# Kernel tuning notes

Measured on AMD Instinct MI355X. Metric: run time of the kernel, lower is better.

The kernel has to match this reference:

```python
import jax, jax.numpy as jnp
import numpy as np
import math

B, T, D = 2, 4096, 1024
H = 16
HEAD_DIM = D // H
CHUNK = 64

def setup_inputs() -> dict:
    key = jax.random.key(0)
    ks = jax.random.split(key, 9)
    s = 1.0 / math.sqrt(D)
    return {
        'x':  jax.random.normal(ks[0], (B, T, D), dtype=jnp.float32),
        'Wq': jax.random.normal(ks[1], (D, D), dtype=jnp.float32) * s,
        'bq': jax.random.normal(ks[2], (D,), dtype=jnp.float32) * 0.01,
        'Wk': jax.random.normal(ks[3], (D, D), dtype=jnp.float32) * s,
        'bk': jax.random.normal(ks[4], (D,), dtype=jnp.float32) * 0.01,
        'Wv': jax.random.normal(ks[5], (D, D), dtype=jnp.float32) * s,
        'bv': jax.random.normal(ks[6], (D,), dtype=jnp.float32) * 0.01,
        'Wo': jax.random.normal(ks[7], (D, D), dtype=jnp.float32) * s,
        'bo': jax.random.normal(ks[8], (D,), dtype=jnp.float32) * 0.01,
    }

def chunked_attention(q, k, v, chunk_size, scale):
    # q,k,v: (B,H,T,hd); causal Q-chunked attention, chunk_size divides T
    Bq, Hq, Tq, hd = q.shape
    S = k.shape[2]
    nc = Tq // chunk_size
    # (nc, B, H, chunk, hd)
    q_chunks = q.reshape(Bq, Hq, nc, chunk_size, hd).transpose(2, 0, 1, 3, 4)
    starts = jnp.arange(nc, dtype=jnp.int32) * chunk_size
    k_pos = jnp.arange(S)

    def body(carry, xs):
        qc, start = xs  # qc: (B,H,chunk,hd)
        scores = jnp.einsum('bhqd,bhkd->bhqk', qc, k) * scale  # (B,H,chunk,S)
        q_pos = start + jnp.arange(chunk_size)
        causal_mask = k_pos[None, :] > q_pos[:, None]  # (chunk,S)
        scores = jnp.where(causal_mask[None, None], -jnp.inf, scores)
        m = jnp.max(scores, axis=-1, keepdims=True)
        m = jnp.where(jnp.isinf(m), jnp.zeros_like(m), m)
        p = jax.nn.softmax(scores - m, axis=-1)
        oc = jnp.einsum('bhqk,bhkd->bhqd', p, v)
        return carry, oc

    _, outs = jax.lax.scan(body, None, (q_chunks, starts))  # (nc,B,H,chunk,hd)
    return outs.transpose(1, 2, 0, 3, 4).reshape(Bq, Hq, Tq, hd)

def reference(x, Wq, bq, Wk, bk, Wv, bv, Wo, bo):
    Bx, Tx, Dx = x.shape
    scale = 1.0 / math.sqrt(HEAD_DIM)

    def proj(W, b):
        y = x @ W.T + b  # torch Linear convention
        return y.reshape(Bx, Tx, H, HEAD_DIM).transpose(0, 2, 1, 3)

    q = proj(Wq, bq)
    k = proj(Wk, bk)
    v = proj(Wv, bv)
    out = chunked_attention(q, k, v, CHUNK, scale)  # (B,H,T,hd)
    out = out.transpose(0, 2, 1, 3).reshape(Bx, Tx, Dx)
    return out @ Wo.T + bo
```

## Files before the change

kernel.cpp:

```cpp
#include <hip/hip_runtime.h>
#include <math.h>

#define B_  2
#define T_  4096
#define D_  1024
#define H_  16
#define HD_ 64
#define M_  8192

using f32x4  = __attribute__((ext_vector_type(4)))  float;
using f32x16 = __attribute__((ext_vector_type(16))) float;
using bfrag  = __attribute__((ext_vector_type(8)))  short;

__device__ __forceinline__ unsigned short f2bf(float f) {
  union { float f; unsigned u; } v; v.f = f;
  unsigned r = v.u + 0x7FFFu + ((v.u >> 16) & 1u);
  return (unsigned short)(r >> 16);
}

__device__ __forceinline__ unsigned cvt_pk(float lo, float hi) {
  unsigned r;
  asm("v_cvt_pk_bf16_f32 %0, %1, %2" : "=v"(r) : "v"(lo), "v"(hi));
  return r;
}

__device__ __forceinline__ void plswap(unsigned &a, unsigned &b) {
  asm("v_permlane32_swap_b32 %0, %1" : "+v"(a), "+v"(b));
}

__device__ __forceinline__ void async16(const void* g, void* l) {
  __builtin_amdgcn_global_load_lds(
      (const __attribute__((address_space(1))) unsigned int*)g,
      (__attribute__((address_space(3))) unsigned int*)l, 16, 0, 0);
}

__global__ __launch_bounds__(256) void convert_all(
    const float* __restrict__ x, const float* __restrict__ wq,
    const float* __restrict__ wk, const float* __restrict__ wv,
    const float* __restrict__ wo, unsigned short* __restrict__ dst)
{
  const size_t NX = (size_t)M_ * D_ / 4;
  const size_t NW = (size_t)D_ * D_ / 4;
  const size_t total = NX + 4 * NW;
  size_t i = (size_t)blockIdx.x * blockDim.x + threadIdx.x;
  size_t stride = (size_t)gridDim.x * blockDim.x;
  for (size_t v = i; v < total; v += stride) {
    const float4* src;
    if (v < NX) {
      src = (const float4*)x + v;
    } else {
      size_t j = v - NX;
      const float* wp = (j < NW) ? wq : (j < 2*NW) ? wk : (j < 3*NW) ? wv : wo;
      src = (const float4*)wp + (j & (NW - 1));
    }
    float4 f = *src;
    ushort4 u;
    u.x = f2bf(f.x); u.y = f2bf(f.y); u.z = f2bf(f.z); u.w = f2bf(f.w);
    *(ushort4*)(dst + v * 4) = u;
  }
}

__global__ __launch_bounds__(256) void gemm_qkv(
    const unsigned short* __restrict__ A,
    const unsigned short* __restrict__ Ww,
    const float* __restrict__ bq, const float* __restrict__ bk,
    const float* __restrict__ bv,
    unsigned short* __restrict__ Qb, unsigned short* __restrict__ Kb,
    unsigned short* __restrict__ Vtb, float qscale)
{
  __shared__ unsigned short a_t[128 * 64];
  __shared__ unsigned short b_t[128 * 64];
  const int tid = threadIdx.x;
  const int lane = tid & 63;
  const int w = tid >> 6;
  const int lo = lane & 15, hi = lane >> 4;
  const int mbase = blockIdx.x * 128;
  const int nbase = blockIdx.y * 128;
  const int wm = w >> 1, wn = w & 1;
  const int K = D_;

  f32x4 acc[4][4];
  #pragma unroll
  for (int m = 0; m < 4; m++)
    #pragma unroll
    for (int n = 0; n < 4; n++) acc[m][n] = f32x4{0.f, 0.f, 0.f, 0.f};

  for (int k0 = 0; k0 < K; k0 += 64) {
    #pragma unroll
    for (int i = 0; i < 4; i++) {
      const int cb = i * 256 + w * 64;
      const int chunk = cb + lane;
      const int row = chunk >> 3, c8 = chunk & 7;
      async16(A  + (size_t)(mbase + row) * K + k0 + c8 * 8, &a_t[cb * 8]);
      async16(Ww + (size_t)(nbase + row) * K + k0 + c8 * 8, &b_t[cb * 8]);
    }
    __syncthreads();
    #pragma unroll
    for (int kk = 0; kk < 2; kk++) {
      bfrag af[4], bf[4];
      #pragma unroll
      for (int m = 0; m < 4; m++)
        af[m] = *(const bfrag*)&a_t[(wm * 64 + m * 16 + lo) * 64 + kk * 32 + hi * 8];
      #pragma unroll
      for (int n = 0; n < 4; n++)
        bf[n] = *(const bfrag*)&b_t[(wn * 64 + n * 16 + lo) * 64 + kk * 32 + hi * 8];
      #pragma unroll
      for (int m = 0; m < 4; m++)
        #pragma unroll
        for (int n = 0; n < 4; n++)
          acc[m][n] = __builtin_amdgcn_mfma_f32_16x16x32_bf16(af[m], bf[n], acc[m][n], 0, 0, 0);
    }
    __syncthreads();
  }

  const int which = nbase >> 10;
  const float* bias = (which == 0) ? bq : (which == 1) ? bk : bv;
  const float osc = (which == 0) ? qscale : 1.0f;
  unsigned short* outp = (which == 0) ? Qb : (which == 1) ? Kb : Vtb;
  const int nloc = nbase & 1023;

  float bvv[4];
  #pragma unroll
  for (int n = 0; n < 4; n++) bvv[n] = bias[nloc + wn * 64 + n * 16 + lo];

  #pragma unroll
  for (int m = 0; m < 4; m++) {
    const int rowl = wm * 64 + m * 16 + hi * 4;
    #pragma unroll
    for (int n = 0; n < 4; n++) {
      const int gn = nloc + wn * 64 + n * 16 + lo;
      const int h = gn >> 6, d = gn & 63;
      #pragma unroll
      for (int i = 0; i < 4; i++) {
        const float v = (acc[m][n][i] + bvv[n]) * osc;
        const int gm = mbase + rowl + i;
        const int b = gm >> 12, t = gm & 4095;
        if (which < 2)
          outp[(((size_t)(b * H_ + h) * T_) + t) * HD_ + d] = f2bf(v);
        else
          outp[(((size_t)(b * H_ + h) * HD_) + d) * T_ + t] = f2bf(v);
      }
    }
  }
}

__global__ __launch_bounds__(256) void gemm_out(
    const unsigned short* __restrict__ A,
    const unsigned short* __restrict__ Bw,
    const float* __restrict__ bias,
    float* __restrict__ out,
    int M, int N, int K)
{
  __shared__ unsigned short a_t[128 * 64];
  __shared__ unsigned short b_t[128 * 64];
  const int tid = threadIdx.x;
  const int lane = tid & 63;
  const int w = tid >> 6;
  const int lo = lane & 15, hi = lane >> 4;
  const int mbase = blockIdx.x * 128;
  const int nbase = blockIdx.y * 128;
  const int wm = w >> 1, wn = w & 1;

  f32x4 acc[4][4];
  #pragma unroll
  for (int m = 0; m < 4; m++)
    #pragma unroll
    for (int n = 0; n < 4; n++) acc[m][n] = f32x4{0.f, 0.f, 0.f, 0.f};

  for (int k0 = 0; k0 < K; k0 += 64) {
    #pragma unroll
    for (int i = 0; i < 4; i++) {
      const int cb = i * 256 + w * 64;
      const int chunk = cb + lane;
      const int row = chunk >> 3, c8 = chunk & 7;
      async16(A  + (size_t)(mbase + row) * K + k0 + c8 * 8, &a_t[cb * 8]);
      async16(Bw + (size_t)(nbase + row) * K + k0 + c8 * 8, &b_t[cb * 8]);
    }
    __syncthreads();
    #pragma unroll
    for (int kk = 0; kk < 2; kk++) {
      bfrag af[4], bf[4];
      #pragma unroll
      for (int m = 0; m < 4; m++)
        af[m] = *(const bfrag*)&a_t[(wm * 64 + m * 16 + lo) * 64 + kk * 32 + hi * 8];
      #pragma unroll
      for (int n = 0; n < 4; n++)
        bf[n] = *(const bfrag*)&b_t[(wn * 64 + n * 16 + lo) * 64 + kk * 32 + hi * 8];
      #pragma unroll
      for (int m = 0; m < 4; m++)
        #pragma unroll
        for (int n = 0; n < 4; n++)
          acc[m][n] = __builtin_amdgcn_mfma_f32_16x16x32_bf16(af[m], bf[n], acc[m][n], 0, 0, 0);
    }
    __syncthreads();
  }

  float bvv[4];
  #pragma unroll
  for (int n = 0; n < 4; n++) bvv[n] = bias[nbase + wn * 64 + n * 16 + lo];

  #pragma unroll
  for (int m = 0; m < 4; m++) {
    const int rowl = wm * 64 + m * 16 + hi * 4;
    #pragma unroll
    for (int n = 0; n < 4; n++) {
      const int gn = nbase + wn * 64 + n * 16 + lo;
      #pragma unroll
      for (int i = 0; i < 4; i++)
        out[(size_t)(mbase + rowl + i) * N + gn] = acc[m][n][i] + bvv[n];
    }
  }
}

__global__ __launch_bounds__(256, 5) void attn_kernel(
    const unsigned short* __restrict__ Qg,
    const unsigned short* __restrict__ Kg,
    const unsigned short* __restrict__ Vtg,
    unsigned short* __restrict__ Og)
{
  __shared__ unsigned short K_lds[2][64 * 64];
  __shared__ unsigned short V_lds[2][64 * 64];
  const int tid = threadIdx.x, lane = tid & 63, w = tid >> 6;
  const int l31 = lane & 31, hi5 = lane >> 5;
  const int bh = blockIdx.x & 31;
  const int qgroup = 63 - (blockIdx.x >> 5);
  const int qhalf = w >> 1, khalf = w & 1;
  const int a = qgroup * 2 + qhalf;
  const int qg_lane = qgroup * 64 + qhalf * 32 + l31;
  const int jmax = qgroup;
  const int jw = (a >= khalf) ? ((a - khalf) >> 1) : -1;
  const int b = bh >> 4, h = bh & 15;

  bfrag qf[4];
  {
    const unsigned short* qp = Qg + ((size_t)bh * T_ + qg_lane) * HD_;
    #pragma unroll
    for (int s = 0; s < 4; s++)
      qf[s] = *(const bfrag*)(qp + s * 16 + hi5 * 8);
  }

  int kidx[4], vidx0[2], vidx1[2];
  {
    const int krow = khalf * 32 + l31;
    #pragma unroll
    for (int s = 0; s < 4; s++)
      kidx[s] = krow * 64 + (((2 * s + hi5) ^ (krow & 7)) * 8);
    #pragma unroll
    for (int s2 = 0; s2 < 2; s2++) {
      vidx0[s2] = l31 * 64 + (((khalf * 4 + s2 * 2 + hi5) ^ (l31 & 7)) * 8);
      vidx1[s2] = (32 + l31) * 64 + (((khalf * 4 + s2 * 2 + hi5) ^ (l31 & 7)) * 8);
    }
  }

  const int row0 = tid >> 3,            sc80 = (tid & 7) ^ (row0 & 7);
  const int row1 = (tid + 256) >> 3,    sc81 = (tid & 7) ^ (row1 & 7);
  const unsigned short* kp0 = Kg  + ((size_t)bh * T_  + row0) * HD_ + sc80 * 8;
  const unsigned short* kp1 = Kg  + ((size_t)bh * T_  + row1) * HD_ + sc81 * 8;
  const unsigned short* vp0 = Vtg + ((size_t)bh * HD_ + row0) * T_  + sc80 * 8;
  const unsigned short* vp1 = Vtg + ((size_t)bh * HD_ + row1) * T_  + sc81 * 8;

  f32x16 o0, o1, zacc;
  #pragma unroll
  for (int r = 0; r < 16; r++) { o0[r] = 0.f; o1[r] = 0.f; zacc[r] = 0.f; }
  float l = 0.f;

  async16(kp0, &K_lds[0][tid * 8]);
  async16(kp1, &K_lds[0][(tid + 256) * 8]);
  async16(vp0, &V_lds[0][tid * 8]);
  async16(vp1, &V_lds[0][(tid + 256) * 8]);
  kp0 += 64 * HD_; kp1 += 64 * HD_; vp0 += 64; vp1 += 64;
  __syncthreads();

  #pragma unroll 2
  for (int j = 0; j <= jmax; ++j) {
    const int buf = j & 1;
    if (j < jmax) {
      async16(kp0, &K_lds[buf ^ 1][tid * 8]);
      async16(kp1, &K_lds[buf ^ 1][(tid + 256) * 8]);
      async16(vp0, &V_lds[buf ^ 1][tid * 8]);
      async16(vp1, &V_lds[buf ^ 1][(tid + 256) * 8]);
      kp0 += 64 * HD_; kp1 += 64 * HD_; vp0 += 64; vp1 += 64;
    }

    if (j <= jw) {
      __builtin_amdgcn_s_setprio(1);
      bfrag kf = *(const bfrag*)&K_lds[buf][kidx[0]];
      f32x16 st = __builtin_amdgcn_mfma_f32_32x32x16_bf16(kf, qf[0], zacc, 0, 0, 0);
      #pragma unroll
      for (int s = 1; s < 4; s++) {
        kf = *(const bfrag*)&K_lds[buf][kidx[s]];
        st = __builtin_amdgcn_mfma_f32_32x32x16_bf16(kf, qf[s], st, 0, 0, 0);
      }
      __builtin_amdgcn_s_setprio(0);

      if (j == jw) {
        const int thr = qg_lane - 64 * j - 32 * khalf - 4 * hi5;
        #pragma unroll
        for (int r = 0; r < 16; r++) {
          const int kl = (r & 3) + 8 * (r >> 2);
          st[r] = (kl > thr) ? -INFINITY : st[r];
        }
      }

      float p16[16];
      #pragma unroll
      for (int r = 0; r < 16; r++) p16[r] = exp2f(st[r]);
      float s8[8];
      #pragma unroll
      for (int r = 0; r < 8; r++) s8[r] = p16[r] + p16[r + 8];
      float rs = ((s8[0] + s8[4]) + (s8[1] + s8[5])) +
                 ((s8[2] + s8[6]) + (s8[3] + s8[7]));
      rs += __shfl_xor(rs, 32);
      l += rs;

      #pragma unroll
      for (int S = 0; S < 2; S++) {
        const int r0 = 8 * S;
        unsigned pk0 = cvt_pk(p16[r0 + 0], p16[r0 + 1]);
        unsigned pk1 = cvt_pk(p16[r0 + 2], p16[r0 + 3]);
        unsigned pk2 = cvt_pk(p16[r0 + 4], p16[r0 + 5]);
        unsigned pk3 = cvt_pk(p16[r0 + 6], p16[r0 + 7]);
        plswap(pk0, pk2);
        plswap(pk1, pk3);
        union { unsigned u[4]; bfrag f; } pb;
        pb.u[0] = pk0; pb.u[1] = pk1; pb.u[2] = pk2; pb.u[3] = pk3;
        __builtin_amdgcn_s_setprio(1);
        bfrag vf0 = *(const bfrag*)&V_lds[buf][vidx0[S]];
        o0 = __builtin_amdgcn_mfma_f32_32x32x16_bf16(vf0, pb.f, o0, 0, 0, 0);
        bfrag vf1 = *(const bfrag*)&V_lds[buf][vidx1[S]];
        o1 = __builtin_amdgcn_mfma_f32_32x32x16_bf16(vf1, pb.f, o1, 0, 0, 0);
        __builtin_amdgcn_s_setprio(0);
      }
    }

    __syncthreads();
  }

  float* sm = (float*)&K_lds[0][0];
  const int moff = (qhalf * 64 + lane) * 17;
  if (khalf) {
    #pragma unroll
    for (int r = 0; r < 16; r++) sm[moff + r] = o0[r];
    sm[moff + 16] = l;
  }
  __syncthreads();
  if (!khalf) {
    #pragma unroll
    for (int r = 0; r < 16; r++) o0[r] += sm[moff + r];
    l += sm[moff + 16];
  }
  __syncthreads();
  if (khalf) {
    #pragma unroll
    for (int r = 0; r < 16; r++) sm[moff + r] = o1[r];
  }
  __syncthreads();
  if (!khalf) {
    #pragma unroll
    for (int r = 0; r < 16; r++) o1[r] += sm[moff + r];
    const float inv = 1.0f / l;
    unsigned short* orow = Og + ((size_t)(b * T_ + qg_lane)) * D_ + h * HD_;
    #pragma unroll
    for (int r = 0; r < 16; r += 2) {
      const int d0 = (r & 3) + 8 * (r >> 2) + 4 * hi5;
      unsigned u0 = cvt_pk(o0[r] * inv, o0[r + 1] * inv);
      unsigned u1 = cvt_pk(o1[r] * inv, o1[r + 1] * inv);
      *(unsigned*)(orow + d0)      = u0;
      *(unsigned*)(orow + 32 + d0) = u1;
    }
  }
}

extern "C" void kernel_launch(void* const* d_in, const int* in_sizes, int n_in,
                              void* d_out, int out_size, void* d_ws, size_t ws_size,
                              hipStream_t stream)
{
  const float* x  = (const float*)d_in[0];
  const float* Wq = (const float*)d_in[1];
  const float* bq = (const float*)d_in[2];
  const float* Wk = (const float*)d_in[3];
  const float* bk = (const float*)d_in[4];
  const float* Wv = (const float*)d_in[5];
  const float* bv = (const float*)d_in[6];
  const float* Wo = (const float*)d_in[7];
  const float* bo = (const float*)d_in[8];

  unsigned short* ws  = (unsigned short*)d_ws;
  unsigned short* xb  = ws;
  unsigned short* wqb = xb  + (size_t)M_ * D_;
  unsigned short* wkb = wqb + (size_t)D_ * D_;
  unsigned short* wvb = wkb + (size_t)D_ * D_;
  unsigned short* wob = wvb + (size_t)D_ * D_;
  unsigned short* Qb  = wob + (size_t)D_ * D_;
  unsigned short* Kb  = Qb  + (size_t)M_ * D_;
  unsigned short* Vtb = Kb  + (size_t)M_ * D_;
  unsigned short* AOb = Vtb + (size_t)M_ * D_;

  convert_all<<<2048, 256, 0, stream>>>(x, Wq, Wk, Wv, Wo, xb);

  const float qscale = 0.125f * 1.44269504f;
  dim3 gq(M_ / 128, 3072 / 128);
  gemm_qkv<<<gq, 256, 0, stream>>>(xb, wqb, bq, bk, bv, Qb, Kb, Vtb, qscale);

  attn_kernel<<<2048, 256, 0, stream>>>(Qb, Kb, Vtb, AOb);

  dim3 go(M_ / 128, D_ / 128);
  gemm_out<<<go, 256, 0, stream>>>(AOb, wob, bo, (float*)d_out, M_, D_, D_);
}
```

Baseline: 253.9 us.

## Load K/V fragments directly from global into registers, dropping LDS staging

The attention kernel no longer stages K and V tiles through double-buffered shared memory with async copies and per-iteration barriers. Each wave now loads its own K and V MFMA fragments straight from global memory into registers, double-buffering K fragments in two register sets. The loop stops at the wave's own causal limit instead of the block-wide limit, and occupancy hints drop from 5 to 3 blocks to make room for the extra registers. This removes LDS traffic and __syncthreads, but trades it for uncoalesced, redundant global/L2 reads, since wave pairs reload the same K/V data and no longer share it through LDS.

Result: slower. 370.2 us (+45.8%).

```diff
diff --git a/kernel.cpp b/kernel.cpp
--- a/kernel.cpp
+++ b/kernel.cpp
@@ -212,14 +212,13 @@
   }
 }
 
-__global__ __launch_bounds__(256, 5) void attn_kernel(
+__global__ __launch_bounds__(256, 3) void attn_kernel(
     const unsigned short* __restrict__ Qg,
     const unsigned short* __restrict__ Kg,
     const unsigned short* __restrict__ Vtg,
     unsigned short* __restrict__ Og)
 {
-  __shared__ unsigned short K_lds[2][64 * 64];
-  __shared__ unsigned short V_lds[2][64 * 64];
+  __shared__ float smrg[2176];
   const int tid = threadIdx.x, lane = tid & 63, w = tid >> 6;
   const int l31 = lane & 31, hi5 = lane >> 5;
   const int bh = blockIdx.x & 31;
@@ -227,137 +226,139 @@
   const int qhalf = w >> 1, khalf = w & 1;
   const int a = qgroup * 2 + qhalf;
   const int qg_lane = qgroup * 64 + qhalf * 32 + l31;
-  const int jmax = qgroup;
   const int jw = (a >= khalf) ? ((a - khalf) >> 1) : -1;
   const int b = bh >> 4, h = bh & 15;
 
-  bfrag qf[4];
+  bfrag qf0, qf1, qf2, qf3;
   {
-    const unsigned short* qp = Qg + ((size_t)bh * T_ + qg_lane) * HD_;
-    #pragma unroll
-    for (int s = 0; s < 4; s++)
-      qf[s] = *(const bfrag*)(qp + s * 16 + hi5 * 8);
-  }
-
-  int kidx[4], vidx0[2], vidx1[2];
-  {
-    const int krow = khalf * 32 + l31;
-    #pragma unroll
-    for (int s = 0; s < 4; s++)
-      kidx[s] = krow * 64 + (((2 * s + hi5) ^ (krow & 7)) * 8);
-    #pragma unroll
-    for (int s2 = 0; s2 < 2; s2++) {
-      vidx0[s2] = l31 * 64 + (((khalf * 4 + s2 * 2 + hi5) ^ (l31 & 7)) * 8);
-      vidx1[s2] = (32 + l31) * 64 + (((khalf * 4 + s2 * 2 + hi5) ^ (l31 & 7)) * 8);
-    }
-  }
-
-  const int row0 = tid >> 3,            sc80 = (tid & 7) ^ (row0 & 7);
-  const int row1 = (tid + 256) >> 3,    sc81 = (tid & 7) ^ (row1 & 7);
-  const unsigned short* kp0 = Kg  + ((size_t)bh * T_  + row0) * HD_ + sc80 * 8;
-  const unsigned short* kp1 = Kg  + ((size_t)bh * T_  + row1) * HD_ + sc81 * 8;
-  const unsigned short* vp0 = Vtg + ((size_t)bh * HD_ + row0) * T_  + sc80 * 8;
-  const unsigned short* vp1 = Vtg + ((size_t)bh * HD_ + row1) * T_  + sc81 * 8;
+    const unsigned short* qp = Qg + ((size_t)bh * T_ + qg_lane) * HD_ + hi5 * 8;
+    qf0 = *(const bfrag*)(qp);
+    qf1 = *(const bfrag*)(qp + 16);
+    qf2 = *(const bfrag*)(qp + 32);
+    qf3 = *(const bfrag*)(qp + 48);
+  }
+
+  const unsigned short* kp =
+      Kg + ((size_t)bh * T_ + khalf * 32 + l31) * HD_ + hi5 * 8;
+  const unsigned short* vp0 =
+      Vtg + ((size_t)bh * HD_ + l31) * T_ + khalf * 32 + hi5 * 8;
+  const unsigned short* vp1 = vp0 + (size_t)32 * T_;
 
   f32x16 o0, o1, zacc;
   #pragma unroll
   for (int r = 0; r < 16; r++) { o0[r] = 0.f; o1[r] = 0.f; zacc[r] = 0.f; }
   float l = 0.f;
 
-  async16(kp0, &K_lds[0][tid * 8]);
-  async16(kp1, &K_lds[0][(tid + 256) * 8]);
-  async16(vp0, &V_lds[0][tid * 8]);
-  async16(vp1, &V_lds[0][(tid + 256) * 8]);
-  kp0 += 64 * HD_; kp1 += 64 * HD_; vp0 += 64; vp1 += 64;
-  __syncthreads();
-
-  #pragma unroll 2
-  for (int j = 0; j <= jmax; ++j) {
-    const int buf = j & 1;
-    if (j < jmax) {
-      async16(kp0, &K_lds[buf ^ 1][tid * 8]);
-      async16(kp1, &K_lds[buf ^ 1][(tid + 256) * 8]);
-      async16(vp0, &V_lds[buf ^ 1][tid * 8]);
-      async16(vp1, &V_lds[buf ^ 1][(tid + 256) * 8]);
-      kp0 += 64 * HD_; kp1 += 64 * HD_; vp0 += 64; vp1 += 64;
-    }
-
-    if (j <= jw) {
-      __builtin_amdgcn_s_setprio(1);
-      bfrag kf = *(const bfrag*)&K_lds[buf][kidx[0]];
-      f32x16 st = __builtin_amdgcn_mfma_f32_32x32x16_bf16(kf, qf[0], zacc, 0, 0, 0);
-      #pragma unroll
-      for (int s = 1; s < 4; s++) {
-        kf = *(const bfrag*)&K_lds[buf][kidx[s]];
-        st = __builtin_amdgcn_mfma_f32_32x32x16_bf16(kf, qf[s], st, 0, 0, 0);
-      }
-      __builtin_amdgcn_s_setprio(0);
-
-      if (j == jw) {
-        const int thr = qg_lane - 64 * j - 32 * khalf - 4 * hi5;
-        #pragma unroll
-        for (int r = 0; r < 16; r++) {
-          const int kl = (r & 3) + 8 * (r >> 2);
-          st[r] = (kl > thr) ? -INFINITY : st[r];
-        }
-      }
-
-      float p16[16];
-      #pragma unroll
-      for (int r = 0; r < 16; r++) p16[r] = exp2f(st[r]);
-      float s8[8];
-      #pragma unroll
-      for (int r = 0; r < 8; r++) s8[r] = p16[r] + p16[r + 8];
-      float rs = ((s8[0] + s8[4]) + (s8[1] + s8[5])) +
-                 ((s8[2] + s8[6]) + (s8[3] + s8[7]));
-      rs += __shfl_xor(rs, 32);
-      l += rs;
-
-      #pragma unroll
-      for (int S = 0; S < 2; S++) {
-        const int r0 = 8 * S;
-        unsigned pk0 = cvt_pk(p16[r0 + 0], p16[r0 + 1]);
-        unsigned pk1 = cvt_pk(p16[r0 + 2], p16[r0 + 3]);
-        unsigned pk2 = cvt_pk(p16[r0 + 4], p16[r0 + 5]);
-        unsigned pk3 = cvt_pk(p16[r0 + 6], p16[r0 + 7]);
-        plswap(pk0, pk2);
-        plswap(pk1, pk3);
-        union { unsigned u[4]; bfrag f; } pb;
-        pb.u[0] = pk0; pb.u[1] = pk1; pb.u[2] = pk2; pb.u[3] = pk3;
-        __builtin_amdgcn_s_setprio(1);
-        bfrag vf0 = *(const bfrag*)&V_lds[buf][vidx0[S]];
-        o0 = __builtin_amdgcn_mfma_f32_32x32x16_bf16(vf0, pb.f, o0, 0, 0, 0);
-        bfrag vf1 = *(const bfrag*)&V_lds[buf][vidx1[S]];
-        o1 = __builtin_amdgcn_mfma_f32_32x32x16_bf16(vf1, pb.f, o1, 0, 0, 0);
-        __builtin_amdgcn_s_setprio(0);
-      }
-    }
-
-    __syncthreads();
-  }
-
-  float* sm = (float*)&K_lds[0][0];
+  bfrag kA0, kA1, kA2, kA3, kB0, kB1, kB2, kB3;
+  bfrag vf00, vf01, vf10, vf11;
+
+  #define LOADK(P) do {                                                      \
+    P##0 = *(const bfrag*)(kp);                                              \
+    P##1 = *(const bfrag*)(kp + 16);                                         \
+    P##2 = *(const bfrag*)(kp + 32);                                         \
+    P##3 = *(const bfrag*)(kp + 48);                                         \
+    kp += (size_t)64 * HD_;                                                  \
+  } while (0)
+
+  #define LOADV() do {                                                       \
+    vf00 = *(const bfrag*)(vp0);                                             \
+    vf01 = *(const bfrag*)(vp0 + 16);                                        \
+    vf10 = *(const bfrag*)(vp1);                                             \
+    vf11 = *(const bfrag*)(vp1 + 16);                                        \
+    vp0 += 64; vp1 += 64;                                                    \
+  } while (0)
+
+  #define COMPUTE(P, J) do {                                                 \
+    __builtin_amdgcn_s_setprio(1);                                           \
+    f32x16 st = __builtin_amdgcn_mfma_f32_32x32x16_bf16(P##0, qf0, zacc, 0, 0, 0); \
+    st = __builtin_amdgcn_mfma_f32_32x32x16_bf16(P##1, qf1, st, 0, 0, 0);    \
+    st = __builtin_amdgcn_mfma_f32_32x32x16_bf16(P##2, qf2, st, 0, 0, 0);    \
+    st = __builtin_amdgcn_mfma_f32_32x32x16_bf16(P##3, qf3, st, 0, 0, 0);    \
+    __builtin_amdgcn_s_setprio(0);                                           \
+    if ((J) == jw) {                                                         \
+      const int thr = qg_lane - 64 * (J) - 32 * khalf - 4 * hi5;             \
+      _Pragma("unroll")                                                      \
+      for (int r = 0; r < 16; r++) {                                         \
+        const int kl = (r & 3) + 8 * (r >> 2);                               \
+        st[r] = (kl > thr) ? -INFINITY : st[r];                              \
+      }                                                                      \
+    }                                                                        \
+    float p16[16];                                                           \
+    _Pragma("unroll")                                                        \
+    for (int r = 0; r < 16; r++) p16[r] = exp2f(st[r]);                      \
+    float s8[8];                                                             \
+    _Pragma("unroll")                                                        \
+    for (int r = 0; r < 8; r++) s8[r] = p16[r] + p16[r + 8];                 \
+    float rs = ((s8[0] + s8[4]) + (s8[1] + s8[5])) +                         \
+               ((s8[2] + s8[6]) + (s8[3] + s8[7]));                          \
+    rs += __shfl_xor(rs, 32);                                                \
+    l += rs;                                                                 \
+    {                                                                        \
+      unsigned pk0 = cvt_pk(p16[0], p16[1]);                                 \
+      unsigned pk1 = cvt_pk(p16[2], p16[3]);                                 \
+      unsigned pk2 = cvt_pk(p16[4], p16[5]);                                 \
+      unsigned pk3 = cvt_pk(p16[6], p16[7]);                                 \
+      plswap(pk0, pk2);                                                      \
+      plswap(pk1, pk3);                                                      \
+      union { unsigned u[4]; bfrag f; } pb;                                  \
+      pb.u[0] = pk0; pb.u[1] = pk1; pb.u[2] = pk2; pb.u[3] = pk3;            \
+      __builtin_amdgcn_s_setprio(1);                                         \
+      o0 = __builtin_amdgcn_mfma_f32_32x32x16_bf16(vf00, pb.f, o0, 0, 0, 0); \
+      o1 = __builtin_amdgcn_mfma_f32_32x32x16_bf16(vf10, pb.f, o1, 0, 0, 0); \
+      __builtin_amdgcn_s_setprio(0);                                         \
+      pk0 = cvt_pk(p16[8], p16[9]);                                          \
+      pk1 = cvt_pk(p16[10], p16[11]);                                        \
+      pk2 = cvt_pk(p16[12], p16[13]);                                        \
+      pk3 = cvt_pk(p16[14], p16[15]);                                        \
+      plswap(pk0, pk2);                                                      \
+      plswap(pk1, pk3);                                                      \
+      pb.u[0] = pk0; pb.u[1] = pk1; pb.u[2] = pk2; pb.u[3] = pk3;            \
+      __builtin_amdgcn_s_setprio(1);                                         \
+      o0 = __builtin_amdgcn_mfma_f32_32x32x16_bf16(vf01, pb.f, o0, 0, 0, 0); \
+      o1 = __builtin_amdgcn_mfma_f32_32x32x16_bf16(vf11, pb.f, o1, 0, 0, 0); \
+      __builtin_amdgcn_s_setprio(0);                                         \
+    }                                                                        \
+  } while (0)
+
+  if (jw >= 0) {
+    LOADK(kA);
+    int j = 0;
+    while (true) {
+      LOADV();
+      if (j < jw) LOADK(kB);
+      COMPUTE(kA, j);
+      ++j; if (j > jw) break;
+      LOADV();
+      if (j < jw) LOADK(kA);
+      COMPUTE(kB, j);
+      ++j; if (j > jw) break;
+    }
+  }
+  #undef LOADK
+  #undef LOADV
+  #undef COMPUTE
+
   const int moff = (qhalf * 64 + lane) * 17;
   if (khalf) {
     #pragma unroll
-    for (int r = 0; r < 16; r++) sm[moff + r] = o0[r];
-    sm[moff + 16] = l;
+    for (int r = 0; r < 16; r++) smrg[moff + r] = o0[r];
+    smrg[moff + 16] = l;
   }
   __syncthreads();
   if (!khalf) {
     #pragma unroll
-    for (int r = 0; r < 16; r++) o0[r] += sm[moff + r];
-    l += sm[moff + 16];
+    for (int r = 0; r < 16; r++) o0[r] += smrg[moff + r];
+    l += smrg[moff + 16];
   }
   __syncthreads();
   if (khalf) {
     #pragma unroll
-    for (int r = 0; r < 16; r++) sm[moff + r] = o1[r];
+    for (int r = 0; r < 16; r++) smrg[moff + r] = o1[r];
   }
   __syncthreads();
   if (!khalf) {
     #pragma unroll
-    for (int r = 0; r < 16; r++) o1[r] += sm[moff + r];
+    for (int r = 0; r < 16; r++) o1[r] += smrg[moff + r];
     const float inv = 1.0f / l;
     unsigned short* orow = Og + ((size_t)(b * T_ + qg_lane)) * D_ + h * HD_;
     #pragma unroll
```
